# Performance work log

Hardware: AMD Instinct MI355X
Metric: run time of the kernel (lower is better)

## Reference

```python
import jax, jax.numpy as jnp
import numpy as np
from jax import lax
from jax.scipy.linalg import solve_triangular

# Newton-Schulz dynamic coefficients (6 iterations), from the source table
NS_COEFFS = [
    (3955/1024, -8306/1024, 5008/1024),
    (3735/1024, -6681/1024, 3463/1024),
    (3799/1024, -6499/1024, 3211/1024),
    (4019/1024, -6385/1024, 2906/1024),
    (2677/1024, -3029/1024, 1162/1024),
    (2172/1024, -1833/1024,  682/1024),
]

B, T, D, H, DK, DV = 4, 1024, 512, 8, 64, 64


def newton_schulz6(M):
    # M: (..., dv, dk), square (dv == dk) so no transpose branch is needed
    X = M / (jnp.linalg.norm(M, axis=(-2, -1), keepdims=True) + 1e-7)
    for a, b, c in NS_COEFFS:
        A = X @ jnp.swapaxes(X, -1, -2)
        Bm = b * A + c * (A @ A)
        X = a * X + Bm @ X
    return X


def setup_inputs() -> dict:
    key = jax.random.key(0)
    ks = jax.random.split(key, 9)
    s = 0.02  # weight init scale
    return {
        "x":  jax.random.normal(ks[0], (B, T, D), jnp.float32),
        "Wq": jax.random.normal(ks[1], (H * DK, D), jnp.float32) * s,
        "Wk": jax.random.normal(ks[2], (H * DK, D), jnp.float32) * s,
        "Wv": jax.random.normal(ks[3], (H * DV, D), jnp.float32) * s,
        "Ww": jax.random.normal(ks[4], (H * DK, D), jnp.float32) * s,
        "Wp": jax.random.normal(ks[5], (H * 2, D), jnp.float32) * s,
        "Wo": jax.random.normal(ks[6], (D, H * DV), jnp.float32) * s,
        "S0": jax.random.normal(ks[7], (H, DV, DK), jnp.float32),
        "M0": jnp.zeros((H, DV, DK), jnp.float32),
    }


def _forward(x, Wq, Wk, Wv, Ww, Wp, Wo, S0, M0):
    b, t, d = x.shape
    h, dv, dk = S0.shape

    def heads(W, e):  # (b,t,d) @ W.T -> (b,h,t,e)
        return (x @ W.T).reshape(b, t, h, e).transpose(0, 2, 1, 3)

    q = heads(Wq, dk)
    k = heads(Wk, dk)
    v = heads(Wv, dv)
    w = heads(Ww, dk)
    p = jax.nn.sigmoid((x @ Wp.T).reshape(b, t, h, 2).transpose(0, 2, 1, 3))
    eta, theta = p[..., 0], p[..., 1]  # (b,h,t)

    # delta-rule redundancy: u_t = v_t - softmax(w_t K_{<t}^T / sqrt(dk)) U_{<t}
    scores = jnp.einsum('bhtd,bhsd->bhts', w, k) / (dk ** 0.5)
    strict = jnp.tril(jnp.ones((t, t), bool), k=-1)  # s < t
    A = jax.nn.softmax(jnp.where(strict, scores, -1e30), axis=-1) * strict
    # (I + A) U = V  (unit lower-triangular solve == the sequential recurrence)
    U = solve_triangular(A, v, lower=True, unit_diagonal=True)  # (b,h,t,dv)

    # sequential state update over time (momentum + Newton-Schulz + S accumulation)
    tm = lambda a: jnp.moveaxis(a, 2, 0)  # time-major
    xs = (tm(U), tm(k), tm(q), jnp.moveaxis(eta, 2, 0), jnp.moveaxis(theta, 2, 0))

    @jax.checkpoint
    def step(carry, inp):
        S, M = carry
        u_t, k_t, q_t, eta_t, theta_t = inp  # (b,h,dv)/(b,h,dk)/(b,h)
        g = u_t[..., :, None] * k_t[..., None, :]        # (b,h,dv,dk)
        th = theta_t[..., None, None]
        M = th * M + (1.0 - th) * g
        Sp = newton_schulz6(M)
        S = S + eta_t[..., None, None] * Sp
        o = jnp.einsum('bhvk,bhk->bhv', S, q_t)
        return (S, M), o

    S_init = jnp.broadcast_to(S0, (b, h, dv, dk))
    M_init = jnp.broadcast_to(M0, (b, h, dv, dk))
    (_, _), O = lax.scan(step, (S_init, M_init), xs)  # O: (t,b,h,dv)

    o = O.transpose(1, 0, 2, 3).reshape(b, t, h * dv)
    return o @ Wo.T  # (b,t,d)


def reference(x, Wq, Wk, Wv, Ww, Wp, Wo, S0, M0):
    return _forward(x, Wq, Wk, Wv, Ww, Wp, Wo, S0, M0)
```

## Files before the change

### kernel.cpp

```cpp
#include <hip/hip_runtime.h>
#include <hip/hip_bf16.h>
#include <math.h>

#define Bn 4
#define Tn 1024
#define Dn 512
#define Hn 8
#define BHn 32
#define LDP 65
#define LDU 68
#define LH 72

typedef _Float16 f16x8 __attribute__((ext_vector_type(8)));
typedef _Float16 f16x4 __attribute__((ext_vector_type(4)));
typedef float    f32x4 __attribute__((ext_vector_type(4)));

__constant__ float NS_Ac[6] = {3955.0f/1024.0f, 3735.0f/1024.0f, 3799.0f/1024.0f,
                               4019.0f/1024.0f, 2677.0f/1024.0f, 2172.0f/1024.0f};
__constant__ float NS_Bc[6] = {-8306.0f/1024.0f, -6681.0f/1024.0f, -6499.0f/1024.0f,
                               -6385.0f/1024.0f, -3029.0f/1024.0f, -1833.0f/1024.0f};
__constant__ float NS_Cc[6] = {5008.0f/1024.0f, 3463.0f/1024.0f, 3211.0f/1024.0f,
                               2906.0f/1024.0f, 1162.0f/1024.0f,  682.0f/1024.0f};

__device__ __forceinline__ f32x4 mfma16(f16x4 a, f16x4 b, f32x4 c) {
  return __builtin_amdgcn_mfma_f32_16x16x16f16(a, b, c, 0, 0, 0);
}
__device__ __forceinline__ f32x4 mfma32(f16x8 a, f16x8 b, f32x4 c) {
  return __builtin_amdgcn_mfma_f32_16x16x32_f16(a, b, c, 0, 0, 0);
}

__device__ __forceinline__ f16x4 cvt4(f32x4 a) {
  f16x4 h;
  h[0] = (_Float16)a[0]; h[1] = (_Float16)a[1];
  h[2] = (_Float16)a[2]; h[3] = (_Float16)a[3];
  return h;
}

__device__ __forceinline__ f16x8 pack8(f16x4 lo, f16x4 hi) {
  f16x8 o;
  o[0] = lo[0]; o[1] = lo[1]; o[2] = lo[2]; o[3] = lo[3];
  o[4] = hi[0]; o[5] = hi[1]; o[6] = hi[2]; o[7] = hi[3];
  return o;
}

__device__ __forceinline__ void set_half(f16x8& v, int h, f16x4 x) {
  if (h) { v[4] = x[0]; v[5] = x[1]; v[6] = x[2]; v[7] = x[3]; }
  else   { v[0] = x[0]; v[1] = x[1]; v[2] = x[2]; v[3] = x[3]; }
}

__device__ __forceinline__ f16x4 get_half(f16x8 v, int h) {
  f16x4 o;
  if (h) { o[0] = v[4]; o[1] = v[5]; o[2] = v[6]; o[3] = v[7]; }
  else   { o[0] = v[0]; o[1] = v[1]; o[2] = v[2]; o[3] = v[3]; }
  return o;
}

__device__ __forceinline__ f16x4 make_If(int r, int g) {
  const int dd = r - 4 * g;
  f16x4 If;
  If[0] = (dd == 0) ? (_Float16)1.f : (_Float16)0.f;
  If[1] = (dd == 1) ? (_Float16)1.f : (_Float16)0.f;
  If[2] = (dd == 2) ? (_Float16)1.f : (_Float16)0.f;
  If[3] = (dd == 3) ? (_Float16)1.f : (_Float16)0.f;
  return If;
}

__device__ __forceinline__ f16x8 ld_frag8(const _Float16* lds, int row, int c, int g) {
  const f16x4 lo = *reinterpret_cast<const f16x4*>(lds + row * LH + (2 * c) * 16 + 4 * g);
  const f16x4 hi = *reinterpret_cast<const f16x4*>(lds + row * LH + (2 * c + 1) * 16 + 4 * g);
  return pack8(lo, hi);
}


__device__ __forceinline__ void stage_tile_h(_Float16* __restrict__ dst,
                                             const float* __restrict__ src,
                                             int srcStride, int tid) {
#pragma unroll
  for (int i = 0; i < 4; ++i) {
    const int idx = tid + (i << 8);
    const int row = idx >> 4;
    const int c4  = (idx & 15) << 2;
    const float4 v = *reinterpret_cast<const float4*>(src + (size_t)row * srcStride + c4);
    f16x4 h;
    h[0] = (_Float16)v.x; h[1] = (_Float16)v.y; h[2] = (_Float16)v.z; h[3] = (_Float16)v.w;
    *reinterpret_cast<f16x4*>(dst + row * LH + c4) = h;
  }
}

__device__ __forceinline__ void stage_tile_u(float* __restrict__ dst,
                                             const float* __restrict__ src, int tid) {
#pragma unroll
  for (int i = 0; i < 4; ++i) {
    const int idx = tid + (i << 8);
    const int row = idx >> 4;
    const int c4  = (idx & 15) << 2;
    *reinterpret_cast<float4*>(dst + row * LDU + c4) =
        *reinterpret_cast<const float4*>(src + (size_t)row * 64 + c4);
  }
}

__device__ __forceinline__ void tri_solve_blocked(const float* __restrict__ Sc,
                                                  float* __restrict__ Ua, int tid) {
  const int dv = tid & 63;
  const int grp = tid >> 6;
#pragma unroll 1
  for (int db = 0; db < 4; ++db) {
    const int base = db * 16;
    if (grp == 0) {
#pragma unroll 1
      for (int rr = 1; rr < 16; ++rr) {
        float s = 0.f;
        for (int c = 0; c < rr; ++c)
          s = fmaf(Sc[(base + rr) * LDP + base + c], Ua[(base + c) * LDU + dv], s);
        Ua[(base + rr) * LDU + dv] -= s;
      }
    }
    __syncthreads();
    if (db < 3) {
      for (int r2 = base + 16 + grp; r2 < 64; r2 += 4) {
        float s = 0.f;
#pragma unroll
        for (int c = 0; c < 16; ++c)
          s = fmaf(Sc[r2 * LDP + base + c], Ua[(base + c) * LDU + dv], s);
        Ua[r2 * LDU + dv] -= s;
      }
    }
    __syncthreads();
  }
}


__global__ __launch_bounds__(256) void proj4_kernel(
    const float* __restrict__ x,
    const float* __restrict__ W0, const float* __restrict__ W1,
    const float* __restrict__ W2, const float* __restrict__ W3,
    float* __restrict__ o0, float* __restrict__ o1,
    float* __restrict__ o2, float* __restrict__ o3) {
  __shared__ __align__(16) _Float16 Af[64 * LH];
  __shared__ __align__(16) _Float16 Bf[64 * LH];
  const float* W; float* outp;
  switch (blockIdx.z) {
    case 0:  W = W0; outp = o0; break;
    case 1:  W = W1; outp = o1; break;
    case 2:  W = W2; outp = o2; break;
    default: W = W3; outp = o3; break;
  }
  const int tid = threadIdx.x;
  const int m0 = blockIdx.x * 64;
  const int n0 = blockIdx.y * 64;
  const int wid = tid >> 6, lane = tid & 63;
  const int r = lane & 15, g = lane >> 4;
  f32x4 acc[4] = {};
  for (int kt = 0; kt < Dn; kt += 64) {
    stage_tile_h(Af, x + (size_t)m0 * Dn + kt, Dn, tid);
    stage_tile_h(Bf, W + (size_t)n0 * Dn + kt, Dn, tid);
    __syncthreads();
    f16x8 a8[2];
#pragma unroll
    for (int c = 0; c < 2; ++c) a8[c] = ld_frag8(Af, 16 * wid + r, c, g);
#pragma unroll
    for (int jb = 0; jb < 4; ++jb) {
#pragma unroll
      for (int c = 0; c < 2; ++c)
        acc[jb] = mfma32(a8[c], ld_frag8(Bf, 16 * jb + r, c, g), acc[jb]);
    }
    __syncthreads();
  }
#pragma unroll
  for (int jb = 0; jb < 4; ++jb)
#pragma unroll
    for (int d = 0; d < 4; ++d) {
      const int m = m0 + 16 * wid + 4 * g + d;
      const int n = n0 + 16 * jb + r;
      const int b = m >> 10, t = m & 1023, h = n >> 6, e = n & 63;
      outp[(((size_t)(b * Hn + h)) * Tn + t) * 64 + e] = acc[jb][d];
    }
}

#define XSTR 516
__global__ __launch_bounds__(256) void wp_kernel(const float* __restrict__ x,
                                                 const float* __restrict__ Wp,
                                                 float* __restrict__ eta,
                                                 float* __restrict__ theta) {
  __shared__ float xs[16 * XSTR];
  __shared__ float wps[16 * XSTR];
  const int tid = threadIdx.x;
  const int r0 = blockIdx.x * 16;
#pragma unroll
  for (int i = 0; i < 8; ++i) {
    const int idx = tid + (i << 8);
    const int r = idx >> 7, c4 = (idx & 127) << 2;
    const float4 v = *reinterpret_cast<const float4*>(x + (size_t)(r0 + r) * Dn + c4);
    float* p = xs + r * XSTR + c4;
    p[0] = v.x; p[1] = v.y; p[2] = v.z; p[3] = v.w;
    const float4 wv = *reinterpret_cast<const float4*>(Wp + (size_t)r * Dn + c4);
    float* pw = wps + r * XSTR + c4;
    pw[0] = wv.x; pw[1] = wv.y; pw[2] = wv.z; pw[3] = wv.w;
  }
  __syncthreads();
  const int row = tid >> 4, col = tid & 15;
  float acc = 0.f;
#pragma unroll 8
  for (int k = 0; k < Dn; ++k) acc = fmaf(xs[row * XSTR + k], wps[col * XSTR + k], acc);
  const float sg = 1.f / (1.f + __expf(-acc));
  const int m = r0 + row, b = m >> 10, t = m & 1023, h = col >> 1;
  float* dst = (col & 1) ? theta : eta;
  dst[((size_t)(b * Hn + h)) * Tn + t] = sg;
}

__global__ __launch_bounds__(256) void rowstats_kernel(
    const float* __restrict__ wb, const float* __restrict__ kb,
    float* __restrict__ rowm, float* __restrict__ rowl) {
  __shared__ __align__(16) _Float16 Wh[64 * LH];
  __shared__ __align__(16) _Float16 Kh[64 * LH];
  const int tb = blockIdx.x, bh = blockIdx.y, t0 = tb * 64;
  const int tid = threadIdx.x, wid = tid >> 6, lane = tid & 63;
  const int r = lane & 15, g = lane >> 4;
  stage_tile_h(Wh, wb + ((size_t)bh * Tn + t0) * 64, 64, tid);
  float rm[4], rl[4];
#pragma unroll
  for (int d = 0; d < 4; ++d) { rm[d] = -INFINITY; rl[d] = 0.f; }
  __syncthreads();
  f16x8 wfr8[2];
#pragma unroll
  for (int c = 0; c < 2; ++c) wfr8[c] = ld_frag8(Wh, 16 * wid + r, c, g);
  for (int sb = 0; sb <= tb; ++sb) {
    __syncthreads();
    stage_tile_h(Kh, kb + ((size_t)bh * Tn + sb * 64) * 64, 64, tid);
    __syncthreads();
    float sv[4][4];
    float tmax[4] = {-INFINITY, -INFINITY, -INFINITY, -INFINITY};
#pragma unroll
    for (int jb = 0; jb < 4; ++jb) {
      f32x4 acc = {0.f, 0.f, 0.f, 0.f};
#pragma unroll
      for (int c = 0; c < 2; ++c)
        acc = mfma32(wfr8[c], ld_frag8(Kh, 16 * jb + r, c, g), acc);
      const int col = sb * 64 + 16 * jb + r;
#pragma unroll
      for (int d = 0; d < 4; ++d) {
        const int row = t0 + 16 * wid + 4 * g + d;
        const float s = (col < row) ? acc[d] * 0.125f : -INFINITY;
        sv[jb][d] = s;
        tmax[d] = fmaxf(tmax[d], s);
      }
    }
#pragma unroll
    for (int m = 1; m < 16; m <<= 1)
#pragma unroll
      for (int d = 0; d < 4; ++d) tmax[d] = fmaxf(tmax[d], __shfl_xor(tmax[d], m, 64));
#pragma unroll
    for (int d = 0; d < 4; ++d) {
      const float mnew  = fmaxf(rm[d], tmax[d]);
      const float msafe = (mnew == -INFINITY) ? 0.f : mnew;
      float s = __expf(sv[0][d] - msafe) + __expf(sv[1][d] - msafe) +
                __expf(sv[2][d] - msafe) + __expf(sv[3][d] - msafe);
#pragma unroll
      for (int m = 1; m < 16; m <<= 1) s += __shfl_xor(s, m, 64);
      const float scale = (rm[d] == -INFINITY) ? 0.f : __expf(rm[d] - msafe);
      rl[d] = rl[d] * scale + s;
      rm[d] = mnew;
    }
  }
  if (r == 0) {
#pragma unroll
    for (int d = 0; d < 4; ++d) {
      const int row = t0 + 16 * wid + 4 * g + d;
      rowm[(size_t)bh * Tn + row] = rm[d];
      rowl[(size_t)bh * Tn + row] = (rl[d] == 0.f) ? 1.f : rl[d];
    }
  }
}

__global__ __launch_bounds__(256) void copyU_kernel(const float* __restrict__ vb,
                                                    float* __restrict__ Ub) {
  const int gid = blockIdx.x * 256 + threadIdx.x;
  ((float4*)Ub)[gid] = ((const float4*)vb)[gid];
}

__global__ __launch_bounds__(256) void solve_diag0_kernel(
    const float* __restrict__ wb, const float* __restrict__ kb,
    const float* __restrict__ vb, const float* __restrict__ rowm,
    const float* __restrict__ rowl, float* __restrict__ Ub) {
  __shared__ __align__(16) _Float16 Wh[64 * LH];
  __shared__ __align__(16) _Float16 Kh[64 * LH];
  __shared__ float Sc[64 * LDP];
  __shared__ __align__(16) float Ua[64 * LDU];
  __shared__ float rmL[64], rlL[64];
  const int bh = blockIdx.x;
  const int tid = threadIdx.x, wid = tid >> 6, lane = tid & 63;
  const int r = lane & 15, g = lane >> 4;
  stage_tile_h(Wh, wb + (size_t)bh * Tn * 64, 64, tid);
  stage_tile_h(Kh, kb + (size_t)bh * Tn * 64, 64, tid);
  stage_tile_u(Ua, vb + (size_t)bh * Tn * 64, tid);
  if (tid < 64) { rmL[tid] = rowm[(size_t)bh * Tn + tid]; rlL[tid] = rowl[(size_t)bh * Tn + tid]; }
  __syncthreads();
  f16x4 wfr[4];
#pragma unroll
  for (int kc = 0; kc < 4; ++kc)
    wfr[kc] = *reinterpret_cast<const f16x4*>(Wh + (16 * wid + r) * LH + kc * 16 + 4 * g);
  float rmv[4], rlv[4];
#pragma unroll
  for (int d = 0; d < 4; ++d) {
    rmv[d] = rmL[16 * wid + 4 * g + d];
    rlv[d] = rlL[16 * wid + 4 * g + d];
  }
#pragma unroll
  for (int jb = 0; jb < 4; ++jb) {
    f32x4 acc = {0.f, 0.f, 0.f, 0.f};
#pragma unroll
    for (int kc = 0; kc < 4; ++kc)
      acc = mfma16(wfr[kc],
                   *reinterpret_cast<const f16x4*>(Kh + (16 * jb + r) * LH + kc * 16 + 4 * g),
                   acc);
#pragma unroll
    for (int d = 0; d < 4; ++d) {
      const int lr = 16 * wid + 4 * g + d, lc = 16 * jb + r;
      Sc[lr * LDP + lc] = (lc < lr) ? __expf(acc[d] * 0.125f - rmv[d]) / rlv[d] : 0.f;
    }
  }
  __syncthreads();
  tri_solve_blocked(Sc, Ua, tid);
#pragma unroll
  for (int i = 0; i < 4; ++i) {
    const int idx = tid + (i << 8);
    const int row = idx >> 4, c4 = (idx & 15) << 2;
    *reinterpret_cast<float4*>(Ub + ((size_t)bh * Tn + row) * 64 + c4) =
        *reinterpret_cast<const float4*>(Ua + row * LDU + c4);
  }
}

__global__ __launch_bounds__(256) void solve_step_kernel(
    const float* __restrict__ wb, const float* __restrict__ kb,
    const float* __restrict__ rowm, const float* __restrict__ rowl,
    float* __restrict__ Ub, int ib) {
  __shared__ __align__(16) _Float16 Wh[64 * LH];
  __shared__ __align__(16) _Float16 Kh[64 * LH];
  __shared__ __align__(16) _Float16 UTh[64 * LH];
  __shared__ float Sc[64 * LDP];
  __shared__ __align__(16) float Ua[64 * LDU];
  __shared__ float rmL[64], rlL[64];
  const int f = ib + 1 + blockIdx.x, bh = blockIdx.y;
  const int tid = threadIdx.x, wid = tid >> 6, lane = tid & 63;
  const int r = lane & 15, g = lane >> 4;
  stage_tile_h(Wh, wb + ((size_t)bh * Tn + f * 64) * 64, 64, tid);
  stage_tile_h(Kh, kb + ((size_t)bh * Tn + ib * 64) * 64, 64, tid);
  {
    const float* src = Ub + ((size_t)bh * Tn + ib * 64) * 64;
#pragma unroll
    for (int i2 = 0; i2 < 4; ++i2) {
      const int idx = tid + (i2 << 8);
      const int row = idx >> 4, c4 = (idx & 15) << 2;
      const float4 v = *reinterpret_cast<const float4*>(src + (size_t)row * 64 + c4);
      UTh[(c4 + 0) * LH + row] = (_Float16)v.x;
      UTh[(c4 + 1) * LH + row] = (_Float16)v.y;
      UTh[(c4 + 2) * LH + row] = (_Float16)v.z;
      UTh[(c4 + 3) * LH + row] = (_Float16)v.w;
    }
  }
  if (tid < 64) {
    rmL[tid] = rowm[(size_t)bh * Tn + f * 64 + tid];
    rlL[tid] = rowl[(size_t)bh * Tn + f * 64 + tid];
  }
  __syncthreads();
  f16x4 wfr[4];
#pragma unroll
  for (int kc = 0; kc < 4; ++kc)
    wfr[kc] = *reinterpret_cast<const f16x4*>(Wh + (16 * wid + r) * LH + kc * 16 + 4 * g);
  float rmv[4], rlv[4];
#pragma unroll
  for (int d = 0; d < 4; ++d) {
    rmv[d] = rmL[16 * wid + 4 * g + d];
    rlv[d] = rlL[16 * wid + 4 * g + d];
  }
  const f16x4 If = make_If(r, g);
  f16x4 Pfr[4];
#pragma unroll
  for (int jb = 0; jb < 4; ++jb) {
    f32x4 acc = {0.f, 0.f, 0.f, 0.f};
#pragma unroll
    for (int kc = 0; kc < 4; ++kc)
      acc = mfma16(wfr[kc],
                   *reinterpret_cast<const f16x4*>(Kh + (16 * jb + r) * LH + kc * 16 + 4 * g),
                   acc);
    f16x4 pf;
#pragma unroll
    for (int d = 0; d < 4; ++d)
      pf[d] = (_Float16)(-__expf(acc[d] * 0.125f - rmv[d]) / rlv[d]);
    Pfr[jb] = cvt4(mfma16(pf, If, (f32x4){0.f, 0.f, 0.f, 0.f}));
  }
  const float* uf = Ub + ((size_t)bh * Tn + f * 64) * 64;
  f32x4 acc2[4];
#pragma unroll
  for (int i = 0; i < 4; ++i) {
    const float4 v = *reinterpret_cast<const float4*>(uf + (size_t)(16 * wid + r) * 64 + 16 * i + 4 * g);
    acc2[i][0] = v.x; acc2[i][1] = v.y; acc2[i][2] = v.z; acc2[i][3] = v.w;
#pragma unroll
    for (int kc = 0; kc < 4; ++kc)
      acc2[i] = mfma16(*reinterpret_cast<const f16x4*>(UTh + (16 * i + r) * LH + kc * 16 + 4 * g),
                       Pfr[kc], acc2[i]);
  }
  if (f == ib + 1) {
    __syncthreads();
    stage_tile_h(Kh, kb + ((size_t)bh * Tn + f * 64) * 64, 64, tid);
#pragma unroll
    for (int i = 0; i < 4; ++i) {
      float4 v = {acc2[i][0], acc2[i][1], acc2[i][2], acc2[i][3]};
      *reinterpret_cast<float4*>(Ua + (16 * wid + r) * LDU + 16 * i + 4 * g) = v;
    }
    __syncthreads();
#pragma unroll
    for (int jb = 0; jb < 4; ++jb) {
      f32x4 acc = {0.f, 0.f, 0.f, 0.f};
#pragma unroll
      for (int kc = 0; kc < 4; ++kc)
        acc = mfma16(wfr[kc],
                     *reinterpret_cast<const f16x4*>(Kh + (16 * jb + r) * LH + kc * 16 + 4 * g),
                     acc);
#pragma unroll
      for (int d = 0; d < 4; ++d) {
        const int lr = 16 * wid + 4 * g + d, lc = 16 * jb + r;
        Sc[lr * LDP + lc] = (lc < lr) ? __expf(acc[d] * 0.125f - rmv[d]) / rlv[d] : 0.f;
      }
    }
    __syncthreads();
    tri_solve_blocked(Sc, Ua, tid);
#pragma unroll
    for (int i2 = 0; i2 < 4; ++i2) {
      const int idx = tid + (i2 << 8);
      const int row = idx >> 4, c4 = (idx & 15) << 2;
      *reinterpret_cast<float4*>(Ub + ((size_t)bh * Tn + f * 64 + row) * 64 + c4) =
          *reinterpret_cast<const float4*>(Ua + row * LDU + c4);
    }
  } else {
#pragma unroll
    for (int i = 0; i < 4; ++i) {
      float4 v = {acc2[i][0], acc2[i][1], acc2[i][2], acc2[i][3]};
      *reinterpret_cast<float4*>(Ub + ((size_t)bh * Tn + f * 64 + 16 * wid + r) * 64 + 16 * i + 4 * g) = v;
    }
  }
}

__global__ __launch_bounds__(256) void mscan_kernel(
    const float* __restrict__ Ub, const float* __restrict__ kb,
    const float* __restrict__ theta, float* __restrict__ Mcarry,
    _Float16* __restrict__ Mbuf, int t0, int Tc) {
  const int gid = blockIdx.x * 256 + threadIdx.x;
  const int bh = gid >> 12, e = gid & 4095;
  const int dv = e >> 6, dk = e & 63;
  float M = Mcarry[gid];
  const float* Urow = Ub + (size_t)bh * Tn * 64;
  const float* krow = kb + (size_t)bh * Tn * 64;
  const float* th   = theta + (size_t)bh * Tn;
  for (int tl = 0; tl < Tc; ++tl) {
    const int t = t0 + tl;
    const float thv = th[t];
    const float g = Urow[(size_t)t * 64 + dv] * krow[(size_t)t * 64 + dk];
    M = thv * M + (1.f - thv) * g;
    Mbuf[((size_t)bh * Tc + tl) * 4096 + e] = (_Float16)M;
  }
  Mcarry[gid] = M;
}

__global__ __launch_bounds__(256, 4) void ns_kernel(_Float16* __restrict__ Mbuf) {
  __shared__ __align__(16) _Float16 Ms[4][64 * LH];
  const int tid  = threadIdx.x;
  const int wid  = tid >> 6, lane = tid & 63;
  const int r    = lane & 15, g = lane >> 4;
  _Float16* src = Mbuf + ((size_t)blockIdx.x * 4 + wid) * 4096;
  _Float16* lds = Ms[wid];
  const int lrow = (lane >> 3), lcol = (lane & 7) * 8;

  float ss = 0.f;
#pragma unroll
  for (int c = 0; c < 8; ++c) {
    const f16x8 h = *reinterpret_cast<const f16x8*>(src + c * 512 + lane * 8);
#pragma unroll
    for (int j = 0; j < 8; ++j) { const float f = (float)h[j]; ss += f * f; }
    *reinterpret_cast<f16x8*>(lds + (c * 8 + lrow) * LH + lcol) = h;
  }
#pragma unroll
  for (int off = 32; off > 0; off >>= 1) ss += __shfl_xor(ss, off, 64);
  const float inv = 1.f / (sqrtf(ss) + 1e-7f);

  f16x8 Xf8[4][2];
#pragma unroll
  for (int i = 0; i < 4; ++i)
#pragma unroll
    for (int c = 0; c < 2; ++c) {
      f16x8 h = ld_frag8(lds, i * 16 + r, c, g);
#pragma unroll
      for (int d = 0; d < 8; ++d) h[d] = (_Float16)((float)h[d] * inv);
      Xf8[i][c] = h;
    }

  const f16x4 If = make_If(r, g);
  f16x4 zero4;
  zero4[0] = (_Float16)0.f; zero4[1] = (_Float16)0.f;
  zero4[2] = (_Float16)0.f; zero4[3] = (_Float16)0.f;
  const f16x8 I8[2] = {pack8(If, zero4), pack8(zero4, If)};
  float Iw[4];
  Iw[0] = (float)If[0]; Iw[1] = (float)If[1]; Iw[2] = (float)If[2]; Iw[3] = (float)If[3];

  f16x8 Ff8[4][2];
  f32x4 acc[4][4];

#pragma unroll 1
  for (int it = 0; it < 6; ++it) {
    const float ca = NS_Ac[it], cb = NS_Bc[it], cc = NS_Cc[it];
#pragma unroll
    for (int i = 0; i < 4; ++i)
#pragma unroll
      for (int j = i; j < 4; ++j) {
        f32x4 a = mfma32(Xf8[i][0], Xf8[j][0], (f32x4){0.f, 0.f, 0.f, 0.f});
        acc[i][j] = mfma32(Xf8[i][1], Xf8[j][1], a);
      }
#pragma unroll
    for (int i = 0; i < 4; ++i) {
      {
        const f16x4 t = cvt4(mfma32(Xf8[i][i >> 1], I8[i & 1], (f32x4){0.f, 0.f, 0.f, 0.f}));
        set_half(Xf8[i][i >> 1], i & 1, t);
      }
#pragma unroll
      for (int j = i + 1; j < 4; ++j) {
        const f16x4 t1 = cvt4(mfma32(Xf8[i][j >> 1], I8[j & 1], (f32x4){0.f, 0.f, 0.f, 0.f}));
        const f16x4 t2 = cvt4(mfma32(Xf8[j][i >> 1], I8[i & 1], (f32x4){0.f, 0.f, 0.f, 0.f}));
        set_half(Xf8[j][i >> 1], i & 1, t1);
        set_half(Xf8[i][j >> 1], j & 1, t2);
      }
    }
#pragma unroll
    for (int i = 0; i < 4; ++i)
#pragma unroll
      for (int j = i; j < 4; ++j) set_half(Ff8[j][i >> 1], i & 1, cvt4(acc[i][j]));
#pragma unroll
    for (int i = 0; i < 4; ++i)
#pragma unroll
      for (int j = i + 1; j < 4; ++j)
        set_half(Ff8[i][j >> 1], j & 1,
                 cvt4(mfma32(Ff8[j][i >> 1], I8[i & 1], (f32x4){0.f, 0.f, 0.f, 0.f})));
    const float bc = cb / cc;
#pragma unroll
    for (int i = 0; i < 4; ++i)
#pragma unroll
      for (int j = i; j < 4; ++j) {
        f32x4 a = acc[i][j];
        a[0] *= bc; a[1] *= bc; a[2] *= bc; a[3] *= bc;
        a = mfma32(Ff8[i][0], Ff8[j][0], a);
        a = mfma32(Ff8[i][1], Ff8[j][1], a);
        a[0] *= cc; a[1] *= cc; a[2] *= cc; a[3] *= cc;
        acc[i][j] = a;
      }
#pragma unroll
    for (int i = 0; i < 4; ++i)
#pragma unroll
      for (int d = 0; d < 4; ++d) acc[i][i][d] = fmaf(ca, Iw[d], acc[i][i][d]);
#pragma unroll
    for (int i = 0; i < 4; ++i)
#pragma unroll
      for (int j = i; j < 4; ++j) set_half(Ff8[j][i >> 1], i & 1, cvt4(acc[i][j]));
#pragma unroll
    for (int i = 0; i < 4; ++i)
#pragma unroll
      for (int j = i + 1; j < 4; ++j)
        set_half(Ff8[i][j >> 1], j & 1,
                 cvt4(mfma32(Ff8[j][i >> 1], I8[i & 1], (f32x4){0.f, 0.f, 0.f, 0.f})));
#pragma unroll
    for (int i = 0; i < 4; ++i)
#pragma unroll
      for (int j = 0; j < 4; ++j) {
        f32x4 a = mfma32(Xf8[i][0], Ff8[j][0], (f32x4){0.f, 0.f, 0.f, 0.f});
        acc[i][j] = mfma32(Xf8[i][1], Ff8[j][1], a);
      }
#pragma unroll
    for (int i = 0; i < 4; ++i)
#pragma unroll
      for (int j = 0; j < 4; ++j)
        set_half(Xf8[j][i >> 1], i & 1, cvt4(acc[i][j]));
  }

#pragma unroll
  for (int i = 0; i < 4; ++i)
#pragma unroll
    for (int c = 0; c < 2; ++c) {
      *reinterpret_cast<f16x4*>(lds + (i * 16 + r) * LH + (2 * c) * 16 + 4 * g) =
          get_half(Xf8[i][c], 0);
      *reinterpret_cast<f16x4*>(lds + (i * 16 + r) * LH + (2 * c + 1) * 16 + 4 * g) =
          get_half(Xf8[i][c], 1);
    }
#pragma unroll
  for (int c = 0; c < 8; ++c) {
    const f16x8 h = *reinterpret_cast<const f16x8*>(lds + (c * 8 + lrow) * LH + lcol);
    *reinterpret_cast<f16x8*>(src + c * 512 + lane * 8) = h;
  }
}

__global__ __launch_bounds__(256) void gsum_kernel(
    const float* __restrict__ eta, const _Float16* __restrict__ Mbuf,
    float* __restrict__ Gbuf, int t0, int Tc) {
  const int j = blockIdx.x, bh = blockIdx.y, tid = threadIdx.x;
  const int nsub = Tc >> 4;
  float acc[16] = {};
#pragma unroll 1
  for (int i = 0; i < 16; ++i) {
    const int tl = j * 16 + i;
    const float ev = eta[(size_t)bh * Tn + t0 + tl];
    const _Float16* sp = Mbuf + ((size_t)bh * Tc + tl) * 4096;
    const f16x8 h0 = *reinterpret_cast<const f16x8*>(sp + tid * 8);
    const f16x8 h1 = *reinterpret_cast<const f16x8*>(sp + 2048 + tid * 8);
#pragma unroll
    for (int u = 0; u < 8; ++u) {
      acc[u]     += ev * (float)h0[u];
      acc[8 + u] += ev * (float)h1[u];
    }
  }
  float* g = Gbuf + ((size_t)bh * nsub + j) * 4096;
#pragma unroll
  for (int u = 0; u < 2; ++u) {
    float4 w0 = {acc[u*4], acc[u*4+1], acc[u*4+2], acc[u*4+3]};
    *reinterpret_cast<float4*>(g + tid * 8 + u * 4) = w0;
    float4 w1 = {acc[8+u*4], acc[8+u*4+1], acc[8+u*4+2], acc[8+u*4+3]};
    *reinterpret_cast<float4*>(g + 2048 + tid * 8 + u * 4) = w1;
  }
}

__global__ __launch_bounds__(256) void sbase_kernel(
    float* __restrict__ Scarry, const float* __restrict__ Gbuf,
    float* __restrict__ Sbase, int Tc) {
  const int gid = blockIdx.x * 256 + threadIdx.x;
  const int bh = gid >> 12, e = gid & 4095;
  const int nsub = Tc >> 4;
  float S = Scarry[gid];
  for (int j = 0; j < nsub; ++j) {
    const size_t idx = ((size_t)bh * nsub + j) * 4096 + e;
    Sbase[idx] = S;
    S += Gbuf[idx];
  }
  Scarry[gid] = S;
}

__global__ __launch_bounds__(256) void outv2_kernel(
    const float* __restrict__ eta, const float* __restrict__ qb,
    const float* __restrict__ Sbase, const _Float16* __restrict__ Mbuf,
    float* __restrict__ ob, int t0, int Tc) {
  const int j = blockIdx.x, bh = blockIdx.y, tid = threadIdx.x;
  const int nsub = Tc >> 4;
  const int ty = tid >> 4, tx = tid & 15;
  const int dv0 = ty * 4, dk0 = tx * 4;
  float S[4][4];
  const float* sb = Sbase + ((size_t)bh * nsub + j) * 4096;
#pragma unroll
  for (int r = 0; r < 4; ++r) {
    const float4 v = *reinterpret_cast<const float4*>(sb + (dv0 + r) * 64 + dk0);
    S[r][0] = v.x; S[r][1] = v.y; S[r][2] = v.z; S[r][3] = v.w;
  }
#pragma unroll 1
  for (int i = 0; i < 16; ++i) {
    const int tl = j * 16 + i, t = t0 + tl;
    const float ev = eta[(size_t)bh * Tn + t];
    const float4 q4 = *reinterpret_cast<const float4*>(qb + ((size_t)bh * Tn + t) * 64 + dk0);
    const _Float16* sp = Mbuf + ((size_t)bh * Tc + tl) * 4096;
    float part[4];
#pragma unroll
    for (int r = 0; r < 4; ++r) {
      const f16x4 h = *reinterpret_cast<const f16x4*>(sp + (dv0 + r) * 64 + dk0);
      S[r][0] += ev * (float)h[0];
      S[r][1] += ev * (float)h[1];
      S[r][2] += ev * (float)h[2];
      S[r][3] += ev * (float)h[3];
      part[r] = S[r][0] * q4.x + S[r][1] * q4.y + S[r][2] * q4.z + S[r][3] * q4.w;
    }
#pragma unroll
    for (int m = 1; m < 16; m <<= 1)
#pragma unroll
      for (int r = 0; r < 4; ++r) part[r] += __shfl_xor(part[r], m, 64);
    if (tx == 0) {
      float4 o4 = {part[0], part[1], part[2], part[3]};
      *reinterpret_cast<float4*>(ob + ((size_t)bh * Tn + t) * 64 + dv0) = o4;
    }
  }
}

__global__ __launch_bounds__(256) void init_carry_kernel(
    const float* __restrict__ S0, const float* __restrict__ M0,
    float* __restrict__ Scarry, float* __restrict__ Mcarry) {
  const int gid = blockIdx.x * 256 + threadIdx.x;
  const int h = (gid >> 12) & 7, e = gid & 4095;
  Scarry[gid] = S0[h * 4096 + e];
  Mcarry[gid] = M0[h * 4096 + e];
}

__global__ __launch_bounds__(256) void out_gemm_kernel(
    const float* __restrict__ ob, const float* __restrict__ Wo,
    float* __restrict__ out) {
  __shared__ __align__(16) _Float16 Af[64 * LH];
  __shared__ __align__(16) _Float16 Bf[64 * LH];
  const int tid = threadIdx.x;
  const int m0 = blockIdx.x * 64;
  const int n0 = blockIdx.y * 64;
  const int wid = tid >> 6, lane = tid & 63;
  const int r = lane & 15, g = lane >> 4;
  f32x4 acc[4] = {};
  for (int kt = 0; kt < Dn; kt += 64) {
    const int h = kt >> 6;
#pragma unroll
    for (int i = 0; i < 4; ++i) {
      const int idx = tid + (i << 8);
      const int row = idx >> 4, c4 = (idx & 15) << 2;
      const int m = m0 + row, b = m >> 10, t = m & 1023;
      const float4 v = *reinterpret_cast<const float4*>(
          ob + ((size_t)(b * Hn + h) * Tn + t) * 64 + c4);
      f16x4 hv;
      hv[0] = (_Float16)v.x; hv[1] = (_Float16)v.y; hv[2] = (_Float16)v.z; hv[3] = (_Float16)v.w;
      *reinterpret_cast<f16x4*>(Af + row * LH + c4) = hv;
    }
    stage_tile_h(Bf, Wo + (size_t)n0 * Dn + kt, Dn, tid);
    __syncthreads();
    f16x8 a8[2];
#pragma unroll
    for (int c = 0; c < 2; ++c) a8[c] = ld_frag8(Af, 16 * wid + r, c, g);
#pragma unroll
    for (int jb = 0; jb < 4; ++jb) {
#pragma unroll
      for (int c = 0; c < 2; ++c)
        acc[jb] = mfma32(a8[c], ld_frag8(Bf, 16 * jb + r, c, g), acc[jb]);
    }
    __syncthreads();
  }
#pragma unroll
  for (int jb = 0; jb < 4; ++jb)
#pragma unroll
    for (int d = 0; d < 4; ++d) {
      const int m = m0 + 16 * wid + 4 * g + d;
      const int n = n0 + 16 * jb + r;
      out[(size_t)m * Dn + n] = acc[jb][d];
    }
}


extern "C" void kernel_launch(void* const* d_in, const int* in_sizes, int n_in,
                              void* d_out, int out_size, void* d_ws, size_t ws_size,
                              hipStream_t stream) {
  (void)in_sizes; (void)n_in; (void)out_size;
  const float* x  = (const float*)d_in[0];
  const float* Wq = (const float*)d_in[1];
  const float* Wk = (const float*)d_in[2];
  const float* Wv = (const float*)d_in[3];
  const float* Ww = (const float*)d_in[4];
  const float* Wp = (const float*)d_in[5];
  const float* Wo = (const float*)d_in[6];
  const float* S0 = (const float*)d_in[7];
  const float* M0 = (const float*)d_in[8];
  float* out = (float*)d_out;
  float* ws  = (float*)d_ws;

  size_t off = 0;
  float* qb  = ws + off; off += (size_t)BHn * Tn * 64;
  float* kb  = ws + off; off += (size_t)BHn * Tn * 64;
  float* vb  = ws + off; off += (size_t)BHn * Tn * 64;
  float* wb  = ws + off; off += (size_t)BHn * Tn * 64;
  float* Ub  = ws + off; off += (size_t)BHn * Tn * 64;
  float* ob  = ws + off; off += (size_t)BHn * Tn * 64;
  float* eta   = ws + off; off += (size_t)BHn * Tn;
  float* theta = ws + off; off += (size_t)BHn * Tn;
  float* rowm  = ws + off; off += (size_t)BHn * Tn;
  float* rowl  = ws + off; off += (size_t)BHn * Tn;
  float* Mcarry = ws + off; off += (size_t)BHn * 4096;
  float* Scarry = ws + off; off += (size_t)BHn * 4096;

  const size_t avail0 = ws_size / sizeof(float) - off;
  int Tc = 256;
  while (Tc > 16 && (size_t)BHn * Tc * 2048 + 2 * (size_t)BHn * (Tc / 16) * 4096 > avail0)
    Tc >>= 1;
  const int nsub = Tc >> 4;

  float* Gbuf  = ws + off; off += (size_t)BHn * nsub * 4096;
  float* Sbase = ws + off; off += (size_t)BHn * nsub * 4096;
  _Float16* Mbuf = (_Float16*)(ws + off);

  hipLaunchKernelGGL(init_carry_kernel, dim3(512), dim3(256), 0, stream, S0, M0, Scarry, Mcarry);
  hipLaunchKernelGGL(proj4_kernel, dim3(64, 8, 4), dim3(256), 0, stream,
                     x, Wq, Wk, Wv, Ww, qb, kb, vb, wb);
  hipLaunchKernelGGL(wp_kernel, dim3(256), dim3(256), 0, stream, x, Wp, eta, theta);
  hipLaunchKernelGGL(rowstats_kernel, dim3(16, 32), dim3(256), 0, stream, wb, kb, rowm, rowl);
  hipLaunchKernelGGL(copyU_kernel, dim3(2048), dim3(256), 0, stream, vb, Ub);
  hipLaunchKernelGGL(solve_diag0_kernel, dim3(32), dim3(256), 0, stream,
                     wb, kb, vb, rowm, rowl, Ub);
  for (int ib = 0; ib < 15; ++ib) {
    hipLaunchKernelGGL(solve_step_kernel, dim3(15 - ib, 32), dim3(256), 0, stream,
                       wb, kb, rowm, rowl, Ub, ib);
  }

  for (int t0 = 0; t0 < Tn; t0 += Tc) {
    hipLaunchKernelGGL(mscan_kernel, dim3(512), dim3(256), 0, stream,
                       Ub, kb, theta, Mcarry, Mbuf, t0, Tc);
    hipLaunchKernelGGL(ns_kernel, dim3(BHn * Tc / 4), dim3(256), 0, stream, Mbuf);
    hipLaunchKernelGGL(gsum_kernel, dim3(nsub, BHn), dim3(256), 0, stream,
                       eta, Mbuf, Gbuf, t0, Tc);
    hipLaunchKernelGGL(sbase_kernel, dim3(512), dim3(256), 0, stream, Scarry, Gbuf, Sbase, Tc);
    hipLaunchKernelGGL(outv2_kernel, dim3(nsub, BHn), dim3(256), 0, stream,
                       eta, qb, Sbase, Mbuf, ob, t0, Tc);
  }

  hipLaunchKernelGGL(out_gemm_kernel, dim3(64, 8), dim3(256), 0, stream, ob, Wo, out);
}
```

Baseline: 1.305 ms.

## Store M buffers in MFMA fragment layout to drop LDS staging in NS kernel

The M buffer, carries and S-base reads are permuted into the MFMA register-fragment order, so the Newton-Schulz kernel loads and stores fragments directly from global memory and no longer round-trips through shared memory. Float-to-half conversions inside the iteration switch to packed round-toward-zero conversion, keeping round-to-nearest only on the final iterate. The time-chunk size is doubled, which halves the number of chunk launches. The risks are extra rounding error from truncation and a larger workspace footprint.

```diff
diff --git a/kernel.cpp b/kernel.cpp
--- a/kernel.cpp
+++ b/kernel.cpp
@@ -36,6 +36,15 @@
   return h;
 }
 
+__device__ __forceinline__ f16x4 cvt4rtz(f32x4 a) {
+  const auto lo = __builtin_amdgcn_cvt_pkrtz(a[0], a[1]);
+  const auto hi = __builtin_amdgcn_cvt_pkrtz(a[2], a[3]);
+  f16x4 h;
+  h[0] = (_Float16)lo[0]; h[1] = (_Float16)lo[1];
+  h[2] = (_Float16)hi[0]; h[3] = (_Float16)hi[1];
+  return h;
+}
+
 __device__ __forceinline__ f16x8 pack8(f16x4 lo, f16x4 hi) {
   f16x8 o;
   o[0] = lo[0]; o[1] = lo[1]; o[2] = lo[2]; o[3] = lo[3];
@@ -46,13 +55,6 @@
 __device__ __forceinline__ void set_half(f16x8& v, int h, f16x4 x) {
   if (h) { v[4] = x[0]; v[5] = x[1]; v[6] = x[2]; v[7] = x[3]; }
   else   { v[0] = x[0]; v[1] = x[1]; v[2] = x[2]; v[3] = x[3]; }
-}
-
-__device__ __forceinline__ f16x4 get_half(f16x8 v, int h) {
-  f16x4 o;
-  if (h) { o[0] = v[4]; o[1] = v[5]; o[2] = v[6]; o[3] = v[7]; }
-  else   { o[0] = v[0]; o[1] = v[1]; o[2] = v[2]; o[3] = v[3]; }
-  return o;
 }
 
 __device__ __forceinline__ f16x4 make_If(int r, int g) {
@@ -70,6 +72,7 @@
   const f16x4 hi = *reinterpret_cast<const f16x4*>(lds + row * LH + (2 * c + 1) * 16 + 4 * g);
   return pack8(lo, hi);
 }
+
 
 
 __device__ __forceinline__ void stage_tile_h(_Float16* __restrict__ dst,
@@ -446,8 +449,12 @@
     const float* __restrict__ theta, float* __restrict__ Mcarry,
     _Float16* __restrict__ Mbuf, int t0, int Tc) {
   const int gid = blockIdx.x * 256 + threadIdx.x;
-  const int bh = gid >> 12, e = gid & 4095;
-  const int dv = e >> 6, dk = e & 63;
+  const int bh = gid >> 12, p = gid & 4095;
+  const int q = p >> 9, i = q >> 1, c = q & 1;
+  const int l = (p >> 3) & 63, g = l >> 4, r = l & 15;
+  const int s = p & 7, jhi = s >> 2, jlo = s & 3;
+  const int dv = i * 16 + r;
+  const int dk = c * 32 + jhi * 16 + g * 4 + jlo;
   float M = Mcarry[gid];
   const float* Urow = Ub + (size_t)bh * Tn * 64;
   const float* krow = kb + (size_t)bh * Tn * 64;
@@ -455,43 +462,41 @@
   for (int tl = 0; tl < Tc; ++tl) {
     const int t = t0 + tl;
     const float thv = th[t];
-    const float g = Urow[(size_t)t * 64 + dv] * krow[(size_t)t * 64 + dk];
-    M = thv * M + (1.f - thv) * g;
-    Mbuf[((size_t)bh * Tc + tl) * 4096 + e] = (_Float16)M;
+    const float gg = Urow[(size_t)t * 64 + dv] * krow[(size_t)t * 64 + dk];
+    M = thv * M + (1.f - thv) * gg;
+    Mbuf[((size_t)bh * Tc + tl) * 4096 + p] = (_Float16)M;
   }
   Mcarry[gid] = M;
 }
 
 __global__ __launch_bounds__(256, 4) void ns_kernel(_Float16* __restrict__ Mbuf) {
-  __shared__ __align__(16) _Float16 Ms[4][64 * LH];
   const int tid  = threadIdx.x;
   const int wid  = tid >> 6, lane = tid & 63;
   const int r    = lane & 15, g = lane >> 4;
   _Float16* src = Mbuf + ((size_t)blockIdx.x * 4 + wid) * 4096;
-  _Float16* lds = Ms[wid];
-  const int lrow = (lane >> 3), lcol = (lane & 7) * 8;
-
+
+  f16x8 Xf8[4][2];
   float ss = 0.f;
 #pragma unroll
-  for (int c = 0; c < 8; ++c) {
-    const f16x8 h = *reinterpret_cast<const f16x8*>(src + c * 512 + lane * 8);
-#pragma unroll
-    for (int j = 0; j < 8; ++j) { const float f = (float)h[j]; ss += f * f; }
-    *reinterpret_cast<f16x8*>(lds + (c * 8 + lrow) * LH + lcol) = h;
-  }
+  for (int i = 0; i < 4; ++i)
+#pragma unroll
+    for (int c = 0; c < 2; ++c) {
+      const f16x8 h = *reinterpret_cast<const f16x8*>(src + (i * 2 + c) * 512 + lane * 8);
+#pragma unroll
+      for (int d = 0; d < 8; ++d) { const float f = (float)h[d]; ss += f * f; }
+      Xf8[i][c] = h;
+    }
 #pragma unroll
   for (int off = 32; off > 0; off >>= 1) ss += __shfl_xor(ss, off, 64);
   const float inv = 1.f / (sqrtf(ss) + 1e-7f);
-
-  f16x8 Xf8[4][2];
 #pragma unroll
   for (int i = 0; i < 4; ++i)
 #pragma unroll
     for (int c = 0; c < 2; ++c) {
-      f16x8 h = ld_frag8(lds, i * 16 + r, c, g);
-#pragma unroll
-      for (int d = 0; d < 8; ++d) h[d] = (_Float16)((float)h[d] * inv);
-      Xf8[i][c] = h;
+      f32x4 lo, hi;
+#pragma unroll
+      for (int d = 0; d < 4; ++d) { lo[d] = (float)Xf8[i][c][d] * inv; hi[d] = (float)Xf8[i][c][d + 4] * inv; }
+      Xf8[i][c] = pack8(cvt4rtz(lo), cvt4rtz(hi));
     }
 
   const f16x4 If = make_If(r, g);
@@ -518,13 +523,13 @@
 #pragma unroll
     for (int i = 0; i < 4; ++i) {
       {
-        const f16x4 t = cvt4(mfma32(Xf8[i][i >> 1], I8[i & 1], (f32x4){0.f, 0.f, 0.f, 0.f}));
+        const f16x4 t = cvt4rtz(mfma32(Xf8[i][i >> 1], I8[i & 1], (f32x4){0.f, 0.f, 0.f, 0.f}));
         set_half(Xf8[i][i >> 1], i & 1, t);
       }
 #pragma unroll
       for (int j = i + 1; j < 4; ++j) {
-        const f16x4 t1 = cvt4(mfma32(Xf8[i][j >> 1], I8[j & 1], (f32x4){0.f, 0.f, 0.f, 0.f}));
-        const f16x4 t2 = cvt4(mfma32(Xf8[j][i >> 1], I8[i & 1], (f32x4){0.f, 0.f, 0.f, 0.f}));
+        const f16x4 t1 = cvt4rtz(mfma32(Xf8[i][j >> 1], I8[j & 1], (f32x4){0.f, 0.f, 0.f, 0.f}));
+        const f16x4 t2 = cvt4rtz(mfma32(Xf8[j][i >> 1], I8[i & 1], (f32x4){0.f, 0.f, 0.f, 0.f}));
         set_half(Xf8[j][i >> 1], i & 1, t1);
         set_half(Xf8[i][j >> 1], j & 1, t2);
       }
@@ -532,13 +537,13 @@
 #pragma unroll
     for (int i = 0; i < 4; ++i)
 #pragma unroll
-      for (int j = i; j < 4; ++j) set_half(Ff8[j][i >> 1], i & 1, cvt4(acc[i][j]));
+      for (int j = i; j < 4; ++j) set_half(Ff8[j][i >> 1], i & 1, cvt4rtz(acc[i][j]));
 #pragma unroll
     for (int i = 0; i < 4; ++i)
 #pragma unroll
       for (int j = i + 1; j < 4; ++j)
         set_half(Ff8[i][j >> 1], j & 1,
-                 cvt4(mfma32(Ff8[j][i >> 1], I8[i & 1], (f32x4){0.f, 0.f, 0.f, 0.f})));
+                 cvt4rtz(mfma32(Ff8[j][i >> 1], I8[i & 1], (f32x4){0.f, 0.f, 0.f, 0.f})));
     const float bc = cb / cc;
 #pragma unroll
     for (int i = 0; i < 4; ++i)
@@ -558,13 +563,13 @@
 #pragma unroll
     for (int i = 0; i < 4; ++i)
 #pragma unroll
-      for (int j = i; j < 4; ++j) set_half(Ff8[j][i >> 1], i & 1, cvt4(acc[i][j]));
+      for (int j = i; j < 4; ++j) set_half(Ff8[j][i >> 1], i & 1, cvt4rtz(acc[i][j]));
 #pragma unroll
     for (int i = 0; i < 4; ++i)
 #pragma unroll
       for (int j = i + 1; j < 4; ++j)
         set_half(Ff8[i][j >> 1], j & 1,
-                 cvt4(mfma32(Ff8[j][i >> 1], I8[i & 1], (f32x4){0.f, 0.f, 0.f, 0.f})));
+                 cvt4rtz(mfma32(Ff8[j][i >> 1], I8[i & 1], (f32x4){0.f, 0.f, 0.f, 0.f})));
 #pragma unroll
     for (int i = 0; i < 4; ++i)
 #pragma unroll
@@ -572,27 +577,19 @@
         f32x4 a = mfma32(Xf8[i][0], Ff8[j][0], (f32x4){0.f, 0.f, 0.f, 0.f});
         acc[i][j] = mfma32(Xf8[i][1], Ff8[j][1], a);
       }
+    const bool last = (it == 5);
 #pragma unroll
     for (int i = 0; i < 4; ++i)
 #pragma unroll
       for (int j = 0; j < 4; ++j)
-        set_half(Xf8[j][i >> 1], i & 1, cvt4(acc[i][j]));
+        set_half(Xf8[j][i >> 1], i & 1, last ? cvt4(acc[i][j]) : cvt4rtz(acc[i][j]));
   }
 
 #pragma unroll
   for (int i = 0; i < 4; ++i)
 #pragma unroll
-    for (int c = 0; c < 2; ++c) {
-      *reinterpret_cast<f16x4*>(lds + (i * 16 + r) * LH + (2 * c) * 16 + 4 * g) =
-          get_half(Xf8[i][c], 0);
-      *reinterpret_cast<f16x4*>(lds + (i * 16 + r) * LH + (2 * c + 1) * 16 + 4 * g) =
-          get_half(Xf8[i][c], 1);
-    }
-#pragma unroll
-  for (int c = 0; c < 8; ++c) {
-    const f16x8 h = *reinterpret_cast<const f16x8*>(lds + (c * 8 + lrow) * LH + lcol);
-    *reinterpret_cast<f16x8*>(src + c * 512 + lane * 8) = h;
-  }
+    for (int c = 0; c < 2; ++c)
+      *reinterpret_cast<f16x8*>(src + (i * 2 + c) * 512 + lane * 8) = Xf8[i][c];
 }
 
 __global__ __launch_bounds__(256) void gsum_kernel(
@@ -647,12 +644,19 @@
   const int nsub = Tc >> 4;
   const int ty = tid >> 4, tx = tid & 15;
   const int dv0 = ty * 4, dk0 = tx * 4;
+  int off[4];
+#pragma unroll
+  for (int r2 = 0; r2 < 4; ++r2) {
+    const int row = dv0 + r2;
+    off[r2] = ((row >> 4) * 2 + (dk0 >> 5)) * 512 +
+              (((dk0 & 15) >> 2) * 16 + (row & 15)) * 8 + ((dk0 >> 4) & 1) * 4;
+  }
   float S[4][4];
   const float* sb = Sbase + ((size_t)bh * nsub + j) * 4096;
 #pragma unroll
-  for (int r = 0; r < 4; ++r) {
-    const float4 v = *reinterpret_cast<const float4*>(sb + (dv0 + r) * 64 + dk0);
-    S[r][0] = v.x; S[r][1] = v.y; S[r][2] = v.z; S[r][3] = v.w;
+  for (int r2 = 0; r2 < 4; ++r2) {
+    const float4 v = *reinterpret_cast<const float4*>(sb + off[r2]);
+    S[r2][0] = v.x; S[r2][1] = v.y; S[r2][2] = v.z; S[r2][3] = v.w;
   }
 #pragma unroll 1
   for (int i = 0; i < 16; ++i) {
@@ -662,18 +666,18 @@
     const _Float16* sp = Mbuf + ((size_t)bh * Tc + tl) * 4096;
     float part[4];
 #pragma unroll
-    for (int r = 0; r < 4; ++r) {
-      const f16x4 h = *reinterpret_cast<const f16x4*>(sp + (dv0 + r) * 64 + dk0);
-      S[r][0] += ev * (float)h[0];
-      S[r][1] += ev * (float)h[1];
-      S[r][2] += ev * (float)h[2];
-      S[r][3] += ev * (float)h[3];
-      part[r] = S[r][0] * q4.x + S[r][1] * q4.y + S[r][2] * q4.z + S[r][3] * q4.w;
+    for (int r2 = 0; r2 < 4; ++r2) {
+      const f16x4 h = *reinterpret_cast<const f16x4*>(sp + off[r2]);
+      S[r2][0] += ev * (float)h[0];
+      S[r2][1] += ev * (float)h[1];
+      S[r2][2] += ev * (float)h[2];
+      S[r2][3] += ev * (float)h[3];
+      part[r2] = S[r2][0] * q4.x + S[r2][1] * q4.y + S[r2][2] * q4.z + S[r2][3] * q4.w;
     }
 #pragma unroll
     for (int m = 1; m < 16; m <<= 1)
 #pragma unroll
-      for (int r = 0; r < 4; ++r) part[r] += __shfl_xor(part[r], m, 64);
+      for (int r2 = 0; r2 < 4; ++r2) part[r2] += __shfl_xor(part[r2], m, 64);
     if (tx == 0) {
       float4 o4 = {part[0], part[1], part[2], part[3]};
       *reinterpret_cast<float4*>(ob + ((size_t)bh * Tn + t) * 64 + dv0) = o4;
@@ -685,7 +689,13 @@
     const float* __restrict__ S0, const float* __restrict__ M0,
     float* __restrict__ Scarry, float* __restrict__ Mcarry) {
   const int gid = blockIdx.x * 256 + threadIdx.x;
-  const int h = (gid >> 12) & 7, e = gid & 4095;
+  const int h = (gid >> 12) & 7, p = gid & 4095;
+  const int q = p >> 9, i = q >> 1, c = q & 1;
+  const int l = (p >> 3) & 63, g = l >> 4, r = l & 15;
+  const int s = p & 7, jhi = s >> 2, jlo = s & 3;
+  const int dv = i * 16 + r;
+  const int dk = c * 32 + jhi * 16 + g * 4 + jlo;
+  const int e = dv * 64 + dk;
   Scarry[gid] = S0[h * 4096 + e];
   Mcarry[gid] = M0[h * 4096 + e];
 }
@@ -769,7 +779,7 @@
   float* Scarry = ws + off; off += (size_t)BHn * 4096;
 
   const size_t avail0 = ws_size / sizeof(float) - off;
-  int Tc = 256;
+  int Tc = 512;
   while (Tc > 16 && (size_t)BHn * Tc * 2048 + 2 * (size_t)BHn * (Tc / 16) * 4096 > avail0)
     Tc >>= 1;
   const int nsub = Tc >> 4;
```

New measurement: 1.307 ms. No clear change (+0.2%).
